# Performance work log

Measured on AMD Instinct MI355X. Metric: run time of the kernel, lower is better.

Reference implementation:

```python
import jax, jax.numpy as jnp
import numpy as np

SR = 48000
N_FFT = 2048
HOP = 64
N_MELS = 128
N_FREQ = N_FFT // 2 + 1  # 1025
N_TARGETS = 64
BATCH = 32
AUDIO_LEN = SR * 1  # duration = 1 s


def _mel_filterbank():
    # torchaudio melscale_fbanks defaults: htk mel scale, norm=None, f_min=0, f_max=sr/2
    freqs = np.linspace(0.0, SR / 2.0, N_FREQ)
    h2m = lambda f: 2595.0 * np.log10(1.0 + f / 700.0)
    m2h = lambda m: 700.0 * (10.0 ** (m / 2595.0) - 1.0)
    m_pts = np.linspace(h2m(0.0), h2m(SR / 2.0), N_MELS + 2)
    f_pts = m2h(m_pts)
    f_diff = np.diff(f_pts)
    slopes = f_pts[None, :] - freqs[:, None]          # [F, n_mels+2]
    down = -slopes[:, :-2] / f_diff[:-1]
    up = slopes[:, 2:] / f_diff[1:]
    fb = np.maximum(0.0, np.minimum(down, up))        # [F, n_mels]
    return fb.astype(np.float32)


def _mel_spec(x, fb):
    # x: [B, L] raw audio -> [B, n_mels, T] power mel spectrogram (power=2, center=True, hann)
    pad = N_FFT // 2
    xp = jnp.pad(x, ((0, 0), (pad, pad)), mode='reflect')
    n_frames = 1 + x.shape[-1] // HOP                 # 751
    idx = jnp.arange(n_frames)[:, None] * HOP + jnp.arange(N_FFT)[None, :]
    frames = xp[:, idx]                               # [B, T, n_fft]
    win = (0.5 * (1.0 - jnp.cos(2.0 * jnp.pi * jnp.arange(N_FFT) / N_FFT))).astype(x.dtype)
    spec = jnp.fft.rfft(frames * win, axis=-1)        # [B, T, F]
    power = spec.real ** 2 + spec.imag ** 2
    return jnp.einsum('btf,fm->bmt', power, fb)       # [B, n_mels, T]


def setup_inputs() -> dict:
    key = jax.random.key(0)
    k1, k2 = jax.random.split(key)
    fb = jnp.asarray(_mel_filterbank())
    x = jax.random.normal(k1, (BATCH, AUDIO_LEN), dtype=jnp.float32) * 0.1
    target_audio = jax.random.normal(k2, (N_TARGETS, AUDIO_LEN), dtype=jnp.float32) * 0.1
    mel_targets = _mel_spec(target_audio, fb)         # [N, n_mels, T]
    return {"x": x, "mel_targets": mel_targets, "mel_fb": fb}


def reference(x, mel_targets, mel_fb):
    m = _mel_spec(x, mel_fb)                          # [B, n_mels, T]
    # mean abs diff of each candidate vs every target: [B, N]
    diffs = jnp.mean(jnp.abs(m[:, None, :, :] - mel_targets[None, :, :, :]), axis=(-1, -2))
    minimums = jnp.min(diffs, axis=-1)                # [B]
    return (minimums,)
```

## Files before the change

### kernel.cpp

```cpp
#include <hip/hip_runtime.h>
#include <math.h>

#define SRATE   48000
#define NFFT    2048
#define N1      1024
#define HOP     64
#define NMELS   128
#define NFREQ   1025
#define NTGT    64
#define BATCH   32
#define NFRAMES 751
#define MELSZ   (NMELS * NFRAMES)
#define NCHUNK  751
#define PADW    132

__device__ __forceinline__ int SP(int a) { return a + 5 * (a >> 5); }
#define SBUF1 1179
__device__ __forceinline__ int TP(int a) { return a + (a >> 5); }
#define TWP   263

__global__ __launch_bounds__(256) void tab_kernel(
    float2* __restrict__ wtab2, float2* __restrict__ gtw) {
  int i = blockIdx.x * 256 + threadIdx.x;
  if (i < N1) {
    float w0 = 0.5f - 0.5f * cosf((float)(2.0 * M_PI / NFFT) * (float)(2 * i));
    float w1 = 0.5f - 0.5f * cosf((float)(2.0 * M_PI / NFFT) * (float)(2 * i + 1));
    wtab2[i] = make_float2(w0, w1);
  }
  if (i <= 1024) {
    float sv, cv;
    sincosf(-(float)(2.0 * M_PI / NFFT) * (float)i, &sv, &cv);
    gtw[i] = make_float2(cv, sv);
  }
}

__global__ __launch_bounds__(256) void fbt_kernel(
    const float* __restrict__ fb, float* __restrict__ fbT,
    int* __restrict__ fs, int* __restrict__ fe) {
  int m = blockIdx.x;
  int tid = threadIdx.x;
  __shared__ int smin[256], smax[256];
  int lmin = NFREQ, lmax = -1;
  for (int f = tid; f < NFREQ; f += 256) {
    float v = fb[f * NMELS + m];
    fbT[m * NFREQ + f] = v;
    if (v > 0.0f) {
      if (f < lmin) lmin = f;
      if (f > lmax) lmax = f;
    }
  }
  smin[tid] = lmin;
  smax[tid] = lmax;
  __syncthreads();
  for (int off = 128; off > 0; off >>= 1) {
    if (tid < off) {
      smin[tid] = min(smin[tid], smin[tid + off]);
      smax[tid] = max(smax[tid], smax[tid + off]);
    }
    __syncthreads();
  }
  if (tid == 0) {
    fs[m] = smin[0];
    fe[m] = smax[0];
  }
}

template<int L>
__device__ __forceinline__ void r4_1024(
    const float2* __restrict__ s, float2* __restrict__ d,
    const float2* __restrict__ tw, int t) {
  constexpr int LOG2L = (L == 1) ? 0 : (L == 4) ? 2 : (L == 16) ? 4
                      : (L == 64) ? 6 : 8;
  constexpr int TS = 256 / L;
  int k = t & (L - 1);
  int j = t >> LOG2L;
  int rb = SP(t);
  float2 u0 = s[rb], u1 = s[rb + 296], u2 = s[rb + 592], u3 = s[rb + 888];
  float a1r, a1i, a2r, a2i, a3r, a3i;
  if (L == 1) {
    a1r = u1.x; a1i = u1.y; a2r = u2.x; a2i = u2.y; a3r = u3.x; a3i = u3.y;
  } else {
    float2 w = tw[TP(k * TS)];
    float wc1 = w.x, ws1 = w.y;
    float wc2 = wc1 * wc1 - ws1 * ws1, ws2 = 2.0f * wc1 * ws1;
    float wc3 = wc2 * wc1 - ws2 * ws1, ws3 = wc2 * ws1 + ws2 * wc1;
    a1r = wc1 * u1.x - ws1 * u1.y; a1i = wc1 * u1.y + ws1 * u1.x;
    a2r = wc2 * u2.x - ws2 * u2.y; a2i = wc2 * u2.y + ws2 * u2.x;
    a3r = wc3 * u3.x - ws3 * u3.y; a3i = wc3 * u3.y + ws3 * u3.x;
  }
  float s0r = u0.x + a2r, s0i = u0.y + a2i;
  float d0r = u0.x - a2r, d0i = u0.y - a2i;
  float s1r = a1r + a3r, s1i = a1i + a3i;
  float d1r = a1r - a3r, d1i = a1i - a3i;
  int wb = (j << (LOG2L + 2)) + k;
  d[SP(wb)]         = make_float2(s0r + s1r, s0i + s1i);
  d[SP(wb + L)]     = make_float2(d0r + d1i, d0i - d1r);
  d[SP(wb + 2 * L)] = make_float2(s0r - s1r, s0i - s1i);
  d[SP(wb + 3 * L)] = make_float2(d0r - d1i, d0i + d1r);
}

__global__ __launch_bounds__(256) void melspec_kernel(
    const float* __restrict__ x, const float* __restrict__ fbT,
    const int* __restrict__ fs, const int* __restrict__ fe,
    const float2* __restrict__ wtab2, const float2* __restrict__ gtw,
    float* __restrict__ mel) {
  __shared__ float2 zA[SBUF1];
  __shared__ float2 zB[SBUF1];
  __shared__ float2 twl[TWP];

  int tid = threadIdx.x;
  int b = blockIdx.x / NFRAMES;
  int t = blockIdx.x - b * NFRAMES;
  const float* xb = x + (size_t)b * SRATE;

  twl[TP(tid)] = gtw[2 * tid];

  int base = t * HOP - NFFT / 2;
  for (int n = tid; n < N1; n += 256) {
    int p0 = base + 2 * n;
    float2 v;
    if (p0 >= 0 && p0 + 1 < SRATE) {
      v = *(const float2*)(xb + p0);
    } else {
      int q0 = p0 < 0 ? -p0 : (p0 >= SRATE ? 2 * SRATE - 2 - p0 : p0);
      int p1 = p0 + 1;
      int q1 = p1 < 0 ? -p1 : (p1 >= SRATE ? 2 * SRATE - 2 - p1 : p1);
      v = make_float2(xb[q0], xb[q1]);
    }
    float2 w2 = wtab2[n];
    zA[SP(n)] = make_float2(v.x * w2.x, v.y * w2.y);
  }
  __syncthreads();

  r4_1024<1>(zA, zB, twl, tid);   __syncthreads();
  r4_1024<4>(zB, zA, twl, tid);   __syncthreads();
  r4_1024<16>(zA, zB, twl, tid);  __syncthreads();
  r4_1024<64>(zB, zA, twl, tid);  __syncthreads();
  r4_1024<256>(zA, zB, twl, tid); __syncthreads();

  float* pw = (float*)zA;
  for (int k = tid; k <= 1024; k += 256) {
    int ka = SP(k & (N1 - 1)), kb = SP((N1 - k) & (N1 - 1));
    float2 Za = zB[ka], Zb = zB[kb];
    float Xer  = 0.5f * (Za.x + Zb.x), Xei = 0.5f * (Za.y - Zb.y);
    float Xor_ = 0.5f * (Za.y + Zb.y), Xoi = 0.5f * (Zb.x - Za.x);
    float2 w = gtw[k];
    float Xr = Xer + w.x * Xor_ - w.y * Xoi;
    float Xi = Xei + w.x * Xoi + w.y * Xor_;
    pw[k] = Xr * Xr + Xi * Xi;
  }
  __syncthreads();

  int m = tid >> 1, half = tid & 1;
  int f0 = fs[m], f1 = fe[m];
  int mid = f0 + ((f1 - f0 + 1) >> 1);
  int lo = half ? mid : f0;
  int hi = half ? f1 : mid - 1;
  const float* col = fbT + (size_t)m * NFREQ;
  float acc = 0.0f;
  for (int f = lo; f <= hi; ++f) acc += pw[f] * col[f];
  acc += __shfl_xor(acc, 1);
  if (!half) mel[(size_t)b * MELSZ + m * NFRAMES + t] = acc;
}

__global__ __launch_bounds__(256) void diff_kernel(
    const float* __restrict__ mel, const float* __restrict__ tgt,
    float* __restrict__ diffs) {
  __shared__ float mel_s[BATCH * PADW];
  __shared__ float tgt_s[NTGT * PADW];
  int tid = threadIdx.x;
  int bg = tid >> 4;
  int kg = tid & 15;
  int c = blockIdx.x;

  for (int q = tid; q < BATCH * 32; q += 256) {
    int row = q >> 5, c4 = q & 31;
    float4 v = *(const float4*)(mel + (size_t)row * MELSZ + c * 128 + c4 * 4);
    *(float4*)(&mel_s[row * PADW + c4 * 4]) = v;
  }
  for (int q = tid; q < NTGT * 32; q += 256) {
    int row = q >> 5, c4 = q & 31;
    float4 v = *(const float4*)(tgt + (size_t)row * MELSZ + c * 128 + c4 * 4);
    *(float4*)(&tgt_s[row * PADW + c4 * 4]) = v;
  }
  __syncthreads();

  float acc[2][4];
  #pragma unroll
  for (int bi = 0; bi < 2; ++bi)
    #pragma unroll
    for (int i = 0; i < 4; ++i) acc[bi][i] = 0.0f;

  for (int j4 = 0; j4 < 32; ++j4) {
    float4 m0 = *(const float4*)(&mel_s[(2 * bg) * PADW + j4 * 4]);
    float4 m1 = *(const float4*)(&mel_s[(2 * bg + 1) * PADW + j4 * 4]);
    #pragma unroll
    for (int i = 0; i < 4; ++i) {
      int k = kg + (i << 4);
      float4 tv = *(const float4*)(&tgt_s[k * PADW + j4 * 4]);
      acc[0][i] += fabsf(m0.x - tv.x) + fabsf(m0.y - tv.y) +
                   fabsf(m0.z - tv.z) + fabsf(m0.w - tv.w);
      acc[1][i] += fabsf(m1.x - tv.x) + fabsf(m1.y - tv.y) +
                   fabsf(m1.z - tv.z) + fabsf(m1.w - tv.w);
    }
  }

  #pragma unroll
  for (int bi = 0; bi < 2; ++bi)
    #pragma unroll
    for (int i = 0; i < 4; ++i)
      atomicAdd(&diffs[(2 * bg + bi) * 64 + kg + (i << 4)], acc[bi][i]);
}

__global__ __launch_bounds__(256) void reduce_kernel(
    const float* __restrict__ diffs, float* __restrict__ out) {
  __shared__ float ds[256];
  int tid = threadIdx.x;
  int p = blockIdx.x * 256 + tid;
  ds[tid] = diffs[p] * (1.0f / (float)MELSZ);
  __syncthreads();
  if (tid < 4) {
    float mn = ds[tid * 64];
    #pragma unroll
    for (int kk = 1; kk < 64; ++kk) mn = fminf(mn, ds[tid * 64 + kk]);
    out[blockIdx.x * 4 + tid] = mn;
  }
}

extern "C" void kernel_launch(void* const* d_in, const int* in_sizes, int n_in,
                              void* d_out, int out_size, void* d_ws, size_t ws_size,
                              hipStream_t stream) {
  const float* x   = (const float*)d_in[0];
  const float* tgt = (const float*)d_in[1];
  const float* fb  = (const float*)d_in[2];
  float* out = (float*)d_out;

  char* ws = (char*)d_ws;
  size_t off = 0;
  float* fbT = (float*)(ws + off);
  off += ((size_t)NMELS * NFREQ * sizeof(float) + 255) & ~(size_t)255;
  int* fs = (int*)(ws + off); off += 1024;
  int* fe = (int*)(ws + off); off += 1024;
  float2* wtab2 = (float2*)(ws + off); off += N1 * sizeof(float2);
  float2* gtw   = (float2*)(ws + off); off += 1056 * sizeof(float2);
  float* mel = (float*)(ws + off);
  off += (size_t)BATCH * MELSZ * sizeof(float);
  float* diffs = (float*)(ws + off); off += 2048 * sizeof(float);

  hipMemsetAsync(diffs, 0, 2048 * sizeof(float), stream);
  tab_kernel<<<8, 256, 0, stream>>>(wtab2, gtw);
  fbt_kernel<<<NMELS, 256, 0, stream>>>(fb, fbT, fs, fe);
  melspec_kernel<<<BATCH * NFRAMES, 256, 0, stream>>>(
      x, fbT, fs, fe, wtab2, gtw, mel);
  diff_kernel<<<NCHUNK, 256, 0, stream>>>(mel, tgt, diffs);
  reduce_kernel<<<8, 256, 0, stream>>>(diffs, out);
}
```

Measured before the change: 241.4 us.

## Restructure STFT as per-wave radix-16 FFT with two frames per block and transposed mel layout

The melspec kernel now processes two frames per 128-thread block, one wavefront each. Each wave computes the 1024-point complex FFT in register-resident radix-16/16/4 passes instead of five LDS-bound radix-4 passes with block-wide barriers. Mel output is written frame-major ([T,128]), and a new transpose kernel reorders the targets into the same layout so diff_kernel still pairs the same elements. This adds a transpose pass over the 64 target spectrograms each call and raises register pressure from 16-element complex arrays.

```diff
diff --git a/kernel.cpp b/kernel.cpp
--- a/kernel.cpp
+++ b/kernel.cpp
@@ -13,11 +13,52 @@
 #define MELSZ   (NMELS * NFRAMES)
 #define NCHUNK  751
 #define PADW    132
-
-__device__ __forceinline__ int SP(int a) { return a + 5 * (a >> 5); }
-#define SBUF1 1179
-__device__ __forceinline__ int TP(int a) { return a + (a >> 5); }
-#define TWP   263
+#define NTILE   376
+
+__device__ __forceinline__ int P2(int a) { return a + (a >> 4); }
+#define ZBUF 1087
+
+__device__ __forceinline__ float2 cmul(float2 a, float2 b) {
+  return make_float2(a.x * b.x - a.y * b.y, a.x * b.y + a.y * b.x);
+}
+
+__device__ __forceinline__ void dft4(float2& x0, float2& x1, float2& x2, float2& x3) {
+  float s0r = x0.x + x2.x, s0i = x0.y + x2.y;
+  float d0r = x0.x - x2.x, d0i = x0.y - x2.y;
+  float s1r = x1.x + x3.x, s1i = x1.y + x3.y;
+  float d1r = x1.x - x3.x, d1i = x1.y - x3.y;
+  x0 = make_float2(s0r + s1r, s0i + s1i);
+  x1 = make_float2(d0r + d1i, d0i - d1r);
+  x2 = make_float2(s0r - s1r, s0i - s1i);
+  x3 = make_float2(d0r - d1i, d0i + d1r);
+}
+
+#define W16_1 make_float2(0.92387953251128674f, -0.38268343236508978f)
+#define W16_2 make_float2(0.70710678118654752f, -0.70710678118654752f)
+#define W16_3 make_float2(0.38268343236508978f, -0.92387953251128674f)
+#define W16_4 make_float2(0.0f, -1.0f)
+#define W16_6 make_float2(-0.70710678118654752f, -0.70710678118654752f)
+#define W16_9 make_float2(-0.92387953251128674f, 0.38268343236508978f)
+
+__device__ __forceinline__ void r16(float2 (&a)[16]) {
+  dft4(a[0], a[4], a[8],  a[12]);
+  dft4(a[1], a[5], a[9],  a[13]);
+  dft4(a[2], a[6], a[10], a[14]);
+  dft4(a[3], a[7], a[11], a[15]);
+  a[5]  = cmul(a[5],  W16_1);
+  a[6]  = cmul(a[6],  W16_2);
+  a[7]  = cmul(a[7],  W16_3);
+  a[9]  = cmul(a[9],  W16_2);
+  a[10] = cmul(a[10], W16_4);
+  a[11] = cmul(a[11], W16_6);
+  a[13] = cmul(a[13], W16_3);
+  a[14] = cmul(a[14], W16_6);
+  a[15] = cmul(a[15], W16_9);
+  dft4(a[0],  a[1],  a[2],  a[3]);
+  dft4(a[4],  a[5],  a[6],  a[7]);
+  dft4(a[8],  a[9],  a[10], a[11]);
+  dft4(a[12], a[13], a[14], a[15]);
+}
 
 __global__ __launch_bounds__(256) void tab_kernel(
     float2* __restrict__ wtab2, float2* __restrict__ gtw) {
@@ -27,7 +68,7 @@
     float w1 = 0.5f - 0.5f * cosf((float)(2.0 * M_PI / NFFT) * (float)(2 * i + 1));
     wtab2[i] = make_float2(w0, w1);
   }
-  if (i <= 1024) {
+  {
     float sv, cv;
     sincosf(-(float)(2.0 * M_PI / NFFT) * (float)i, &sv, &cv);
     gtw[i] = make_float2(cv, sv);
@@ -65,58 +106,52 @@
   }
 }
 
-template<int L>
-__device__ __forceinline__ void r4_1024(
-    const float2* __restrict__ s, float2* __restrict__ d,
-    const float2* __restrict__ tw, int t) {
-  constexpr int LOG2L = (L == 1) ? 0 : (L == 4) ? 2 : (L == 16) ? 4
-                      : (L == 64) ? 6 : 8;
-  constexpr int TS = 256 / L;
-  int k = t & (L - 1);
-  int j = t >> LOG2L;
-  int rb = SP(t);
-  float2 u0 = s[rb], u1 = s[rb + 296], u2 = s[rb + 592], u3 = s[rb + 888];
-  float a1r, a1i, a2r, a2i, a3r, a3i;
-  if (L == 1) {
-    a1r = u1.x; a1i = u1.y; a2r = u2.x; a2i = u2.y; a3r = u3.x; a3i = u3.y;
-  } else {
-    float2 w = tw[TP(k * TS)];
-    float wc1 = w.x, ws1 = w.y;
-    float wc2 = wc1 * wc1 - ws1 * ws1, ws2 = 2.0f * wc1 * ws1;
-    float wc3 = wc2 * wc1 - ws2 * ws1, ws3 = wc2 * ws1 + ws2 * wc1;
-    a1r = wc1 * u1.x - ws1 * u1.y; a1i = wc1 * u1.y + ws1 * u1.x;
-    a2r = wc2 * u2.x - ws2 * u2.y; a2i = wc2 * u2.y + ws2 * u2.x;
-    a3r = wc3 * u3.x - ws3 * u3.y; a3i = wc3 * u3.y + ws3 * u3.x;
-  }
-  float s0r = u0.x + a2r, s0i = u0.y + a2i;
-  float d0r = u0.x - a2r, d0i = u0.y - a2i;
-  float s1r = a1r + a3r, s1i = a1i + a3i;
-  float d1r = a1r - a3r, d1i = a1i - a3i;
-  int wb = (j << (LOG2L + 2)) + k;
-  d[SP(wb)]         = make_float2(s0r + s1r, s0i + s1i);
-  d[SP(wb + L)]     = make_float2(d0r + d1i, d0i - d1r);
-  d[SP(wb + 2 * L)] = make_float2(s0r - s1r, s0i - s1i);
-  d[SP(wb + 3 * L)] = make_float2(d0r - d1i, d0i + d1r);
-}
-
-__global__ __launch_bounds__(256) void melspec_kernel(
+__global__ __launch_bounds__(256) void tpose_kernel(
+    const float* __restrict__ tgt, float* __restrict__ tgtT) {
+  __shared__ float tile[32][33];
+  int k = blockIdx.z;
+  int mt = blockIdx.y;
+  int tt = blockIdx.x;
+  int tx = threadIdx.x & 31, ty = threadIdx.x >> 5;
+  const float* src = tgt + (size_t)k * MELSZ;
+  float* dst = tgtT + (size_t)k * MELSZ;
+  #pragma unroll
+  for (int r = 0; r < 4; ++r) {
+    int m = mt * 32 + ty + r * 8;
+    int t = tt * 32 + tx;
+    if (t < NFRAMES) tile[ty + r * 8][tx] = src[m * NFRAMES + t];
+  }
+  __syncthreads();
+  #pragma unroll
+  for (int r = 0; r < 4; ++r) {
+    int t = tt * 32 + ty + r * 8;
+    int m = mt * 32 + tx;
+    if (t < NFRAMES) dst[t * 128 + m] = tile[tx][ty + r * 8];
+  }
+}
+
+__global__ __launch_bounds__(128) void melspec_kernel(
     const float* __restrict__ x, const float* __restrict__ fbT,
     const int* __restrict__ fs, const int* __restrict__ fe,
     const float2* __restrict__ wtab2, const float2* __restrict__ gtw,
     float* __restrict__ mel) {
-  __shared__ float2 zA[SBUF1];
-  __shared__ float2 zB[SBUF1];
-  __shared__ float2 twl[TWP];
+  __shared__ float2 z[2][2][ZBUF];
 
   int tid = threadIdx.x;
-  int b = blockIdx.x / NFRAMES;
-  int t = blockIdx.x - b * NFRAMES;
+  int bi = blockIdx.x;
+  int b = bi / NTILE;
+  int tile = bi - b * NTILE;
+  int wv = tid >> 6, l = tid & 63;
+  int t = tile * 2 + wv;
+  int tc = t < NFRAMES ? t : NFRAMES - 1;
   const float* xb = x + (size_t)b * SRATE;
-
-  twl[TP(tid)] = gtw[2 * tid];
-
-  int base = t * HOP - NFFT / 2;
-  for (int n = tid; n < N1; n += 256) {
+  float2* A  = z[wv][0];
+  float2* Bb = z[wv][1];
+
+  int base = tc * HOP - NFFT / 2;
+  #pragma unroll
+  for (int m = 0; m < 16; ++m) {
+    int n = l + (m << 6);
     int p0 = base + 2 * n;
     float2 v;
     if (p0 >= 0 && p0 + 1 < SRATE) {
@@ -128,20 +163,56 @@
       v = make_float2(xb[q0], xb[q1]);
     }
     float2 w2 = wtab2[n];
-    zA[SP(n)] = make_float2(v.x * w2.x, v.y * w2.y);
-  }
-  __syncthreads();
-
-  r4_1024<1>(zA, zB, twl, tid);   __syncthreads();
-  r4_1024<4>(zB, zA, twl, tid);   __syncthreads();
-  r4_1024<16>(zA, zB, twl, tid);  __syncthreads();
-  r4_1024<64>(zB, zA, twl, tid);  __syncthreads();
-  r4_1024<256>(zA, zB, twl, tid); __syncthreads();
-
-  float* pw = (float*)zA;
-  for (int k = tid; k <= 1024; k += 256) {
-    int ka = SP(k & (N1 - 1)), kb = SP((N1 - k) & (N1 - 1));
-    float2 Za = zB[ka], Zb = zB[kb];
+    A[P2(n)] = make_float2(v.x * w2.x, v.y * w2.y);
+  }
+  __syncthreads();
+
+  float2 a[16];
+
+  #pragma unroll
+  for (int m = 0; m < 16; ++m) a[m] = A[P2(l + (m << 6))];
+  r16(a);
+  #pragma unroll
+  for (int s = 0; s < 4; ++s)
+    #pragma unroll
+    for (int q = 0; q < 4; ++q)
+      Bb[P2(16 * l + s + 4 * q)] = a[q + 4 * s];
+  __syncthreads();
+
+  {
+    int k2 = l & 15, j2 = l >> 4;
+    #pragma unroll
+    for (int m = 0; m < 16; ++m) a[m] = Bb[P2(l + (m << 6))];
+    #pragma unroll
+    for (int m = 1; m < 16; ++m) a[m] = cmul(a[m], gtw[8 * k2 * m]);
+    r16(a);
+    int wb = j2 * 256 + k2;
+    #pragma unroll
+    for (int s = 0; s < 4; ++s)
+      #pragma unroll
+      for (int q = 0; q < 4; ++q)
+        A[P2(wb + 16 * (s + 4 * q))] = a[q + 4 * s];
+  }
+  __syncthreads();
+
+  #pragma unroll
+  for (int g = 0; g < 4; ++g) {
+    int t3 = l + (g << 6);
+    float2 u0 = A[P2(t3)],       u1 = A[P2(t3 + 256)];
+    float2 u2 = A[P2(t3 + 512)], u3 = A[P2(t3 + 768)];
+    u1 = cmul(u1, gtw[2 * t3]);
+    u2 = cmul(u2, gtw[4 * t3]);
+    u3 = cmul(u3, gtw[6 * t3]);
+    dft4(u0, u1, u2, u3);
+    A[P2(t3)] = u0;       A[P2(t3 + 256)] = u1;
+    A[P2(t3 + 512)] = u2; A[P2(t3 + 768)] = u3;
+  }
+  __syncthreads();
+
+  float* pw = (float*)Bb;
+  for (int k = l; k <= 1024; k += 64) {
+    int ka = P2(k & (N1 - 1)), kb = P2((N1 - k) & (N1 - 1));
+    float2 Za = A[ka], Zb = A[kb];
     float Xer  = 0.5f * (Za.x + Zb.x), Xei = 0.5f * (Za.y - Zb.y);
     float Xor_ = 0.5f * (Za.y + Zb.y), Xoi = 0.5f * (Zb.x - Za.x);
     float2 w = gtw[k];
@@ -151,20 +222,23 @@
   }
   __syncthreads();
 
-  int m = tid >> 1, half = tid & 1;
+  int m = tid;
   int f0 = fs[m], f1 = fe[m];
-  int mid = f0 + ((f1 - f0 + 1) >> 1);
-  int lo = half ? mid : f0;
-  int hi = half ? f1 : mid - 1;
   const float* col = fbT + (size_t)m * NFREQ;
-  float acc = 0.0f;
-  for (int f = lo; f <= hi; ++f) acc += pw[f] * col[f];
-  acc += __shfl_xor(acc, 1);
-  if (!half) mel[(size_t)b * MELSZ + m * NFRAMES + t] = acc;
+  #pragma unroll
+  for (int p = 0; p < 2; ++p) {
+    int tt = tile * 2 + p;
+    if (tt < NFRAMES) {
+      const float* pwf = (const float*)z[p][1];
+      float acc = 0.0f;
+      for (int f = f0; f <= f1; ++f) acc += pwf[f] * col[f];
+      mel[(size_t)b * MELSZ + (size_t)tt * 128 + m] = acc;
+    }
+  }
 }
 
 __global__ __launch_bounds__(256) void diff_kernel(
-    const float* __restrict__ mel, const float* __restrict__ tgt,
+    const float* __restrict__ mel, const float* __restrict__ tgtT,
     float* __restrict__ diffs) {
   __shared__ float mel_s[BATCH * PADW];
   __shared__ float tgt_s[NTGT * PADW];
@@ -180,7 +254,7 @@
   }
   for (int q = tid; q < NTGT * 32; q += 256) {
     int row = q >> 5, c4 = q & 31;
-    float4 v = *(const float4*)(tgt + (size_t)row * MELSZ + c * 128 + c4 * 4);
+    float4 v = *(const float4*)(tgtT + (size_t)row * MELSZ + c * 128 + c4 * 4);
     *(float4*)(&tgt_s[row * PADW + c4 * 4]) = v;
   }
   __syncthreads();
@@ -242,16 +316,19 @@
   int* fs = (int*)(ws + off); off += 1024;
   int* fe = (int*)(ws + off); off += 1024;
   float2* wtab2 = (float2*)(ws + off); off += N1 * sizeof(float2);
-  float2* gtw   = (float2*)(ws + off); off += 1056 * sizeof(float2);
+  float2* gtw   = (float2*)(ws + off); off += 2048 * sizeof(float2);
   float* mel = (float*)(ws + off);
   off += (size_t)BATCH * MELSZ * sizeof(float);
+  float* tgtT = (float*)(ws + off);
+  off += (size_t)NTGT * MELSZ * sizeof(float);
   float* diffs = (float*)(ws + off); off += 2048 * sizeof(float);
 
   hipMemsetAsync(diffs, 0, 2048 * sizeof(float), stream);
   tab_kernel<<<8, 256, 0, stream>>>(wtab2, gtw);
   fbt_kernel<<<NMELS, 256, 0, stream>>>(fb, fbT, fs, fe);
-  melspec_kernel<<<BATCH * NFRAMES, 256, 0, stream>>>(
+  tpose_kernel<<<dim3(24, 4, NTGT), 256, 0, stream>>>(tgt, tgtT);
+  melspec_kernel<<<BATCH * NTILE, 128, 0, stream>>>(
       x, fbT, fs, fe, wtab2, gtw, mel);
-  diff_kernel<<<NCHUNK, 256, 0, stream>>>(mel, tgt, diffs);
+  diff_kernel<<<NCHUNK, 256, 0, stream>>>(mel, tgtT, diffs);
   reduce_kernel<<<8, 256, 0, stream>>>(diffs, out);
 }
```

New measurement: 392.8 us. 62.7% more time.
